# Kernel optimization log

Hardware: AMD Instinct MI355X
Metric: run time of the kernel (lower is better)

The kernel has to match this reference:

```python
import jax, jax.numpy as jnp
import numpy as np

NUM_LAYERS = 5
EMB_DIM = 300
NUM_ATOM_TYPE = 121
NUM_CHIRALITY = 11
NUM_BOND_TYPE = 7
NUM_BOND_DIR = 3
BN_EPS = 1e-5


def setup_inputs() -> dict:
    key = jax.random.key(0)
    ks = jax.random.split(key, 16)
    N, E, D, L = 100000, 200000, EMB_DIM, NUM_LAYERS

    def glorot(k, shape):
        fan_in, fan_out = shape[-2], shape[-1]
        s = jnp.sqrt(6.0 / (fan_in + fan_out))
        return jax.random.uniform(k, shape, jnp.float32, -s, s)

    x = jax.random.randint(ks[0], (N, 2), 0, 11)  # atom type / chirality (both < 11, in range)
    edge_index = jax.random.randint(ks[1], (2, E), 0, N)
    edge_attr = jax.random.randint(ks[2], (E, 2), 0, 3)

    return {
        "x": x,
        "edge_index": edge_index,
        "edge_attr": edge_attr,
        "x_emb1": glorot(ks[3], (NUM_ATOM_TYPE, D)),
        "x_emb2": glorot(ks[4], (NUM_CHIRALITY, D)),
        "edge_emb1": glorot(ks[5], (L, NUM_BOND_TYPE, D)),
        "edge_emb2": glorot(ks[6], (L, NUM_BOND_DIR, D)),
        "w1": glorot(ks[7], (L, D, 2 * D)),
        "b1": jnp.zeros((L, 2 * D), jnp.float32),
        "w2": glorot(ks[8], (L, 2 * D, D)),
        "b2": jnp.zeros((L, D), jnp.float32),
        "bn_gamma": jnp.ones((L, D), jnp.float32),
        "bn_beta": jnp.zeros((L, D), jnp.float32),
    }


def reference(x, edge_index, edge_attr, x_emb1, x_emb2, edge_emb1, edge_emb2,
              w1, b1, w2, b2, bn_gamma, bn_beta):
    N = x.shape[0]
    # GINConv.forward adds self loops with edge_attr row [4, 0]
    loop = jnp.arange(N)
    src = jnp.concatenate([edge_index[0], loop])  # [E+N]
    dst = jnp.concatenate([edge_index[1], loop])  # [E+N]
    ea0 = jnp.concatenate([edge_attr[:, 0], jnp.full((N,), 4, edge_attr.dtype)])
    ea1 = jnp.concatenate([edge_attr[:, 1], jnp.zeros((N,), edge_attr.dtype)])

    # node input embedding
    h = x_emb1[x[:, 0]] + x_emb2[x[:, 1]]  # [N, D]

    for l in range(NUM_LAYERS):
        # edge embeddings (incl. self loops)
        eemb = edge_emb1[l][ea0] + edge_emb2[l][ea1]  # [E+N, D]
        # message: x_j + edge_attr, aggr='add' at destination nodes
        msg = h[src] + eemb
        agg = jax.ops.segment_sum(msg, dst, num_segments=N)  # [N, D]
        # GIN update MLP: Linear(D, 2D) -> ReLU -> Linear(2D, D)
        h2 = jax.nn.relu(agg @ w1[l] + b1[l]) @ w2[l] + b2[l]
        # BatchNorm1d (training mode: batch statistics, biased variance)
        mean = h2.mean(axis=0)
        var = h2.var(axis=0)
        h2 = (h2 - mean) * jax.lax.rsqrt(var + BN_EPS) * bn_gamma[l] + bn_beta[l]
        # ReLU on all but last layer (dropout is identity, drop_ratio=0)
        if l < NUM_LAYERS - 1:
            h2 = jax.nn.relu(h2)
        h = h2
    # JK == 'last'
    return h
```

## Files before the change

### kernel.cpp

```cpp
#include <hip/hip_runtime.h>
#include <hip/hip_bf16.h>
#include <stdint.h>

typedef __bf16 bf16_t;
typedef bf16_t bf16x8 __attribute__((ext_vector_type(8)));
typedef bf16_t bf16x4 __attribute__((ext_vector_type(4)));
typedef float  f32x4  __attribute__((ext_vector_type(4)));

__global__ void embed_kernel(const int* __restrict__ x, const float* __restrict__ e1,
                             const float* __restrict__ e2, bf16_t* __restrict__ h, int N) {
  const int w = (blockIdx.x * blockDim.x + threadIdx.x) >> 6;
  const int lane = threadIdx.x & 63;
  if (w >= N || lane >= 40) return;
  const int t0 = x[2 * w], t1 = x[2 * w + 1];
  const int co = lane * 8;
  f32x4 a0 = *(const f32x4*)&e1[t0 * 300 + co];
  f32x4 a1 = *(const f32x4*)&e1[t0 * 300 + co + 4];
  f32x4 b0 = *(const f32x4*)&e2[t1 * 300 + co];
  f32x4 b1 = *(const f32x4*)&e2[t1 * 300 + co + 4];
  bf16x8 o;
  #pragma unroll
  for (int j = 0; j < 8; j++) {
    float v = (j < 4) ? (a0[j] + b0[j]) : (a1[j - 4] + b1[j - 4]);
    o[j] = (co + j < 300) ? (bf16_t)v : (bf16_t)0.f;
  }
  *(bf16x8*)&h[(size_t)w * 320 + co] = o;
}

__global__ void count_deg_kernel(const int* __restrict__ ei, int* __restrict__ deg, int E) {
  int e = blockIdx.x * 256 + threadIdx.x;
  if (e < E) atomicAdd(&deg[ei[E + e]], 1);
}

__global__ void scan_partial_kernel(const int* __restrict__ deg, int* __restrict__ part, int N) {
  __shared__ int s[256];
  const int tid = threadIdx.x;
  const int idx = blockIdx.x * 256 + tid;
  s[tid] = (idx < N) ? deg[idx] : 0;
  __syncthreads();
  for (int off = 128; off > 0; off >>= 1) {
    if (tid < off) s[tid] += s[tid + off];
    __syncthreads();
  }
  if (tid == 0) part[blockIdx.x] = s[0];
}

__global__ void scan_block_kernel(int* __restrict__ part, int n) {
  __shared__ int s[1024];
  const int tid = threadIdx.x;
  const int v = (tid < n) ? part[tid] : 0;
  s[tid] = v;
  __syncthreads();
  for (int off = 1; off < 1024; off <<= 1) {
    int x = (tid >= off) ? s[tid - off] : 0;
    __syncthreads();
    s[tid] += x;
    __syncthreads();
  }
  if (tid < n) part[tid] = s[tid] - v;
}

__global__ void scan_final_kernel(const int* __restrict__ deg, const int* __restrict__ part,
                                  int* __restrict__ rowptr, int* __restrict__ cursor, int N, int E) {
  __shared__ int s[256];
  const int tid = threadIdx.x;
  const int idx = blockIdx.x * 256 + tid;
  const int v = (idx < N) ? deg[idx] : 0;
  s[tid] = v;
  __syncthreads();
  for (int off = 1; off < 256; off <<= 1) {
    int x = (tid >= off) ? s[tid - off] : 0;
    __syncthreads();
    s[tid] += x;
    __syncthreads();
  }
  if (idx < N) {
    int ex = s[tid] - v + part[blockIdx.x];
    rowptr[idx] = ex;
    cursor[idx] = ex;
  }
  if (idx == 0) rowptr[N] = E;
}

__global__ void fill_csr_kernel(const int* __restrict__ ei, const int* __restrict__ ea,
                                int* __restrict__ cursor, int* __restrict__ epack, int E) {
  int e = blockIdx.x * 256 + threadIdx.x;
  if (e >= E) return;
  int slot = atomicAdd(&cursor[ei[E + e]], 1);
  int a = ea[2 * e] * 3 + ea[2 * e + 1];
  epack[slot] = (ei[e] & 0xFFFFF) | (a << 20);
}

__global__ void convert_w1_kernel(const float* __restrict__ w1, bf16_t* __restrict__ o) {
  int id = blockIdx.x * 256 + threadIdx.x;
  if (id >= 5 * 40 * 10 * 512) return;
  int j = id & 7;
  int lane = (id >> 3) & 63;
  int rest = id >> 9;
  int ks = rest % 10;
  int nt = (rest / 10) % 40;
  int l = rest / 400;
  int ml = lane & 15, quad = lane >> 4;
  int n = nt * 16 + ml;
  int k = ks * 32 + quad * 8 + j;
  float v = (k < 300 && n < 600) ? w1[((size_t)l * 300 + k) * 600 + n] : 0.f;
  o[id] = (bf16_t)v;
}

__global__ void convert_w2_kernel(const float* __restrict__ w2, bf16_t* __restrict__ o) {
  int id = blockIdx.x * 256 + threadIdx.x;
  if (id >= 5 * 24 * 20 * 512) return;
  int j = id & 7;
  int lane = (id >> 3) & 63;
  int rest = id >> 9;
  int ks = rest % 20;
  int nt = (rest / 20) % 24;
  int l = rest / 480;
  int ml = lane & 15, quad = lane >> 4;
  int n = nt * 16 + ml;
  int k = ks * 32 + quad * 8 + j;
  float v = (k < 600 && n < 300) ? w2[((size_t)l * 600 + k) * 300 + n] : 0.f;
  o[id] = (bf16_t)v;
}

__global__ void pad_bias_kernel(const float* __restrict__ b1, const float* __restrict__ b2,
                                float* __restrict__ b1p, float* __restrict__ b2p) {
  int t = blockIdx.x * 256 + threadIdx.x;
  if (t < 5 * 640) {
    int l = t / 640, n = t % 640;
    b1p[t] = (n < 600) ? b1[l * 600 + n] : 0.f;
  }
  if (t < 5 * 384) {
    int l = t / 384, n = t % 384;
    b2p[t] = (n < 300) ? b2[l * 300 + n] : 0.f;
  }
}

__global__ void build_t12_kernel(const float* __restrict__ ee1, const float* __restrict__ ee2,
                                 bf16_t* __restrict__ T12) {
  int id = blockIdx.x * 256 + threadIdx.x;
  if (id >= 5 * 21 * 320) return;
  int col = id % 320;
  int r = id / 320;
  int l = r / 21;
  int a = r % 21;
  int a0 = a / 3, a1 = a % 3;
  float v = 0.f;
  if (col < 300) v = ee1[((size_t)l * 7 + a0) * 300 + col] + ee2[((size_t)l * 3 + a1) * 300 + col];
  T12[id] = (bf16_t)v;
}

template <bool FUSE_BN>
__global__ void aggregate_kernel(const bf16_t* __restrict__ hsrc, const int* __restrict__ rowptr,
                                 const int* __restrict__ epack, const bf16_t* __restrict__ T12L,
                                 const float* __restrict__ scale, const float* __restrict__ shift,
                                 bf16_t* __restrict__ agg, int N, int LDH) {
  const int g = blockIdx.x * 256 + threadIdx.x;
  const int w = g / 40;
  if (w >= N) return;
  const int co = (g - w * 40) * 8;

  float sc[8], sh[8];
  if (FUSE_BN) {
    f32x4 s0 = *(const f32x4*)&scale[co];
    f32x4 s1 = *(const f32x4*)&scale[co + 4];
    f32x4 t0 = *(const f32x4*)&shift[co];
    f32x4 t1 = *(const f32x4*)&shift[co + 4];
    #pragma unroll
    for (int j = 0; j < 4; j++) { sc[j] = s0[j]; sc[j + 4] = s1[j]; sh[j] = t0[j]; sh[j + 4] = t1[j]; }
  }

  const int beg = rowptr[w], end = rowptr[w + 1];
  float acc[8];
  {
    bf16x8 hv = *(const bf16x8*)&hsrc[(size_t)w * LDH + co];
    bf16x8 tv = *(const bf16x8*)&T12L[12 * 320 + co];
    #pragma unroll
    for (int j = 0; j < 8; j++) {
      float v = (float)hv[j];
      if (FUSE_BN) v = fmaxf(v * sc[j] + sh[j], 0.f);
      acc[j] = v + (float)tv[j];
    }
  }
  for (int e = beg; e < end; e++) {
    const int p = epack[e];
    const int s = p & 0xFFFFF;
    const int a = (p >> 20) & 0x1F;
    bf16x8 hv = *(const bf16x8*)&hsrc[(size_t)s * LDH + co];
    bf16x8 tv = *(const bf16x8*)&T12L[a * 320 + co];
    #pragma unroll
    for (int j = 0; j < 8; j++) {
      float v = (float)hv[j];
      if (FUSE_BN) v = fmaxf(v * sc[j] + sh[j], 0.f);
      acc[j] += v + (float)tv[j];
    }
  }
  bf16x8 o;
  #pragma unroll
  for (int j = 0; j < 8; j++) o[j] = (bf16_t)acc[j];
  *(bf16x8*)&agg[(size_t)w * 320 + co] = o;
}

__global__ __launch_bounds__(512) void fused_mlp_kernel(
    const bf16_t* __restrict__ agg,
    const bf16_t* __restrict__ W1f,
    const bf16_t* __restrict__ W2f,
    const float* __restrict__ b1p,
    const float* __restrict__ b2p,
    bf16_t* __restrict__ H2,
    float* __restrict__ sums, float* __restrict__ sumsq, int Nvalid) {
  __shared__ __align__(16) bf16_t As[10 * 64 * 32];
  __shared__ __align__(16) bf16_t C1p[64 * 136];

  const int tid = threadIdx.x;
  const int lane = tid & 63;
  const int w = tid >> 6;
  const int ml = lane & 15, quad = lane >> 4;
  const int kx = (ml >> 1) & 3;
  const size_t bm = (size_t)blockIdx.x * 64;

  #pragma unroll
  for (int it = 0; it < 5; it++) {
    const int s = it * 512 + tid;
    const int ks = s >> 8;
    const int u = s & 255;
    const int row = u >> 2;
    const int cg = (u & 3) ^ ((u >> 3) & 3);
    bf16x8 v = *(const bf16x8*)&agg[(bm + row) * 320 + ks * 32 + cg * 8];
    *(bf16x8*)&As[(size_t)s * 8] = v;
  }
  asm volatile("s_waitcnt lgkmcnt(0)" ::: "memory");
  __builtin_amdgcn_s_barrier();

  f32x4 acc1[4];
  f32x4 acc2[4][3];
  #pragma unroll
  for (int mf = 0; mf < 4; mf++)
    #pragma unroll
    for (int nf = 0; nf < 3; nf++) acc2[mf][nf] = (f32x4){0.f, 0.f, 0.f, 0.f};

  auto phase1 = [&](int c) {
    #pragma unroll
    for (int mt = 0; mt < 4; mt++) acc1[mt] = (f32x4){0.f, 0.f, 0.f, 0.f};
    const bf16_t* wp = W1f + (((size_t)(c * 8 + w) * 10) * 64 + lane) * 8;
    #pragma unroll
    for (int ks = 0; ks < 10; ks++) {
      bf16x8 w1f = *(const bf16x8*)(wp + (size_t)ks * 512);
      #pragma unroll
      for (int mt = 0; mt < 4; mt++) {
        bf16x8 aF = *(const bf16x8*)&As[((ks * 64 + mt * 16 + ml) * 4 + (quad ^ kx)) * 8];
        acc1[mt] = __builtin_amdgcn_mfma_f32_16x16x32_bf16(w1f, aF, acc1[mt], 0, 0, 0);
      }
    }
  };

  phase1(0);

  for (int c = 0; c < 5; c++) {
    {
      const int nloc = w * 16 + quad * 4;
      f32x4 bv = *(const f32x4*)&b1p[c * 128 + nloc];
      #pragma unroll
      for (int mt = 0; mt < 4; mt++) {
        bf16x4 o;
        #pragma unroll
        for (int i = 0; i < 4; i++) {
          float v = acc1[mt][i] + bv[i];
          o[i] = (bf16_t)fmaxf(v, 0.f);
        }
        *(bf16x4*)&C1p[(mt * 16 + ml) * 136 + nloc] = o;
      }
    }
    asm volatile("s_waitcnt lgkmcnt(0)" ::: "memory");
    __builtin_amdgcn_s_barrier();

    #pragma unroll
    for (int ks2 = 0; ks2 < 4; ks2++) {
      bf16x8 c1f[4];
      #pragma unroll
      for (int mf = 0; mf < 4; mf++)
        c1f[mf] = *(const bf16x8*)&C1p[(mf * 16 + ml) * 136 + ks2 * 32 + quad * 8];
      #pragma unroll
      for (int nf = 0; nf < 3; nf++) {
        bf16x8 w2f = *(const bf16x8*)&W2f[(((size_t)(w * 3 + nf) * 20 + c * 4 + ks2) * 64 + lane) * 8];
        #pragma unroll
        for (int mf = 0; mf < 4; mf++)
          acc2[mf][nf] = __builtin_amdgcn_mfma_f32_16x16x32_bf16(c1f[mf], w2f, acc2[mf][nf], 0, 0, 0);
      }
    }
    if (c < 4) phase1(c + 1);
    asm volatile("s_waitcnt lgkmcnt(0)" ::: "memory");
    __builtin_amdgcn_s_barrier();
  }

  #pragma unroll
  for (int nf = 0; nf < 3; nf++) {
    const int colg = (w * 3 + nf) * 16 + ml;
    const float bv = b2p[colg];
    float s = 0.f, sq = 0.f;
    #pragma unroll
    for (int mf = 0; mf < 4; mf++) {
      #pragma unroll
      for (int i = 0; i < 4; i++) {
        const size_t rowg = bm + mf * 16 + quad * 4 + i;
        float v = acc2[mf][nf][i] + bv;
        H2[rowg * 384 + colg] = (bf16_t)v;
        const bool ok = rowg < (size_t)Nvalid;
        s += ok ? v : 0.f;
        sq += ok ? v * v : 0.f;
      }
    }
    s += __shfl_down(s, 16);
    sq += __shfl_down(sq, 16);
    s += __shfl_down(s, 32);
    sq += __shfl_down(sq, 32);
    if (quad == 0) {
      atomicAdd(&sums[colg], s);
      atomicAdd(&sumsq[colg], sq);
    }
  }
}

__global__ void bn_params_kernel(const float* __restrict__ sums, const float* __restrict__ sumsq,
                                 const float* __restrict__ gamma, const float* __restrict__ beta,
                                 float* __restrict__ scale, float* __restrict__ shift, int N) {
  const int col = threadIdx.x;
  if (col >= 384) return;
  if (col >= 300) {
    scale[col] = 0.f;
    shift[col] = 0.f;
    return;
  }
  const float inv = 1.f / (float)N;
  const float mean = sums[col] * inv;
  float var = sumsq[col] * inv - mean * mean;
  if (var < 0.f) var = 0.f;
  const float sc = gamma[col] * rsqrtf(var + 1e-5f);
  scale[col] = sc;
  shift[col] = beta[col] - mean * sc;
}

__global__ void bn_apply_kernel(const bf16_t* __restrict__ H2, const float* __restrict__ scale,
                                const float* __restrict__ shift, float* __restrict__ out, int N) {
  const int w = (blockIdx.x * blockDim.x + threadIdx.x) >> 6;
  const int lane = threadIdx.x & 63;
  if (w >= N || lane >= 40) return;
  const int co = lane * 8;
  bf16x8 v8 = *(const bf16x8*)&H2[(size_t)w * 384 + co];
  f32x4 s0 = *(const f32x4*)&scale[co];
  f32x4 s1 = *(const f32x4*)&scale[co + 4];
  f32x4 t0 = *(const f32x4*)&shift[co];
  f32x4 t1 = *(const f32x4*)&shift[co + 4];
  #pragma unroll
  for (int j = 0; j < 8; j++) {
    float sc = (j < 4) ? s0[j] : s1[j - 4];
    float sh = (j < 4) ? t0[j] : t1[j - 4];
    float v = (float)v8[j] * sc + sh;
    if (co + j < 300) out[(size_t)w * 300 + co + j] = v;
  }
}

extern "C" void kernel_launch(void* const* d_in, const int* in_sizes, int n_in,
                              void* d_out, int out_size, void* d_ws, size_t ws_size,
                              hipStream_t stream) {
  const int* x = (const int*)d_in[0];
  const int* ei = (const int*)d_in[1];
  const int* ea = (const int*)d_in[2];
  const float* xe1 = (const float*)d_in[3];
  const float* xe2 = (const float*)d_in[4];
  const float* ee1 = (const float*)d_in[5];
  const float* ee2 = (const float*)d_in[6];
  const float* w1 = (const float*)d_in[7];
  const float* b1 = (const float*)d_in[8];
  const float* w2 = (const float*)d_in[9];
  const float* b2 = (const float*)d_in[10];
  const float* gam = (const float*)d_in[11];
  const float* bet = (const float*)d_in[12];

  const int N = in_sizes[0] / 2;
  const int E = in_sizes[1] / 2;
  const int Mt = (N + 127) / 128;
  const size_t Mp = (size_t)Mt * 128;
  const int Mt2 = (int)(Mp / 64);

  char* p = (char*)d_ws;
  auto take = [&](size_t b) -> char* {
    char* r = p;
    p += (b + 255) & ~(size_t)255;
    return r;
  };
  bf16_t* h    = (bf16_t*)take(Mp * 320 * 2);
  bf16_t* agg  = (bf16_t*)take(Mp * 320 * 2);
  bf16_t* H2   = (bf16_t*)take(Mp * 384 * 2);
  bf16_t* W1f  = (bf16_t*)take((size_t)5 * 40 * 10 * 512 * 2);
  bf16_t* W2f  = (bf16_t*)take((size_t)5 * 24 * 20 * 512 * 2);
  bf16_t* T12  = (bf16_t*)take((size_t)5 * 21 * 320 * 2);
  float* b1p   = (float*)take((size_t)5 * 640 * 4);
  float* b2p   = (float*)take((size_t)5 * 384 * 4);
  int* deg     = (int*)take((size_t)N * 4);
  int* rowptr  = (int*)take((size_t)(N + 1) * 4);
  int* cursor  = (int*)take((size_t)N * 4);
  int* part    = (int*)take(1024 * 4);
  int* epack   = (int*)take((size_t)E * 4);
  float* sums  = (float*)take(384 * 4);
  float* sumsq = (float*)take(384 * 4);
  float* scale = (float*)take(384 * 4);
  float* shift = (float*)take(384 * 4);

  hipMemsetAsync(agg, 0, Mp * 320 * 2, stream);
  hipMemsetAsync(deg, 0, (size_t)N * 4, stream);

  const int nwb = (N + 3) / 4;
  embed_kernel<<<nwb, 256, 0, stream>>>(x, xe1, xe2, h, N);

  count_deg_kernel<<<(E + 255) / 256, 256, 0, stream>>>(ei, deg, E);
  const int nsb = (N + 255) / 256;
  scan_partial_kernel<<<nsb, 256, 0, stream>>>(deg, part, N);
  scan_block_kernel<<<1, 1024, 0, stream>>>(part, nsb);
  scan_final_kernel<<<nsb, 256, 0, stream>>>(deg, part, rowptr, cursor, N, E);
  fill_csr_kernel<<<(E + 255) / 256, 256, 0, stream>>>(ei, ea, cursor, epack, E);

  convert_w1_kernel<<<(5 * 40 * 10 * 512 + 255) / 256, 256, 0, stream>>>(w1, W1f);
  convert_w2_kernel<<<(5 * 24 * 20 * 512 + 255) / 256, 256, 0, stream>>>(w2, W2f);
  pad_bias_kernel<<<(5 * 640 + 255) / 256, 256, 0, stream>>>(b1, b2, b1p, b2p);
  build_t12_kernel<<<(5 * 21 * 320 + 255) / 256, 256, 0, stream>>>(ee1, ee2, T12);

  const int nab = (N * 40 + 255) / 256;

  for (int l = 0; l < 5; l++) {
    if (l == 0) {
      aggregate_kernel<false><<<nab, 256, 0, stream>>>(h, rowptr, epack,
                                                       T12 + (size_t)l * 21 * 320,
                                                       scale, shift, agg, N, 320);
    } else {
      aggregate_kernel<true><<<nab, 256, 0, stream>>>(H2, rowptr, epack,
                                                      T12 + (size_t)l * 21 * 320,
                                                      scale, shift, agg, N, 384);
    }
    hipMemsetAsync(sums, 0, 384 * 4, stream);
    hipMemsetAsync(sumsq, 0, 384 * 4, stream);
    fused_mlp_kernel<<<Mt2, 512, 0, stream>>>(
        agg, W1f + (size_t)l * 40 * 10 * 512, W2f + (size_t)l * 24 * 20 * 512,
        b1p + (size_t)l * 640, b2p + (size_t)l * 384, H2, sums, sumsq, N);
    bn_params_kernel<<<1, 384, 0, stream>>>(sums, sumsq, gam + (size_t)l * 300,
                                            bet + (size_t)l * 300, scale, shift, N);
  }
  bn_apply_kernel<<<nwb, 256, 0, stream>>>(H2, scale, shift, (float*)d_out, N);
}
```

Measured before the change: 1.384 ms.

## Double-buffer MLP hidden tile and retile phase1 with XOR-swizzled LDS

The fused MLP kernel now keeps two hidden-activation buffers in LDS, so phase1 for chunk c+1 writes one buffer while phase2 reads the other. This removes one barrier per chunk. Phase1 is retiled so each wave computes a 2x2 block of 16x16 tiles (two row groups by four column groups), which reuses each W1 fragment load across two A fragments. The padded C1 layout is replaced with an XOR swizzle to avoid LDS bank conflicts, and launch bounds now request 4 waves per SIMD. The second buffer adds LDS, and the occupancy hint may cause register spills.

After: 1.300 ms. -6.1%, faster.

```diff
diff --git a/kernel.cpp b/kernel.cpp
--- a/kernel.cpp
+++ b/kernel.cpp
@@ -201,7 +201,7 @@
   *(bf16x8*)&agg[(size_t)w * 320 + co] = o;
 }
 
-__global__ __launch_bounds__(512) void fused_mlp_kernel(
+__global__ __launch_bounds__(512, 4) void fused_mlp_kernel(
     const bf16_t* __restrict__ agg,
     const bf16_t* __restrict__ W1f,
     const bf16_t* __restrict__ W2f,
@@ -210,13 +210,16 @@
     bf16_t* __restrict__ H2,
     float* __restrict__ sums, float* __restrict__ sumsq, int Nvalid) {
   __shared__ __align__(16) bf16_t As[10 * 64 * 32];
-  __shared__ __align__(16) bf16_t C1p[64 * 136];
+  __shared__ __align__(16) bf16_t C1pA[64 * 128];
+  __shared__ __align__(16) bf16_t C1pB[64 * 128];
 
   const int tid = threadIdx.x;
   const int lane = tid & 63;
   const int w = tid >> 6;
   const int ml = lane & 15, quad = lane >> 4;
   const int kx = (ml >> 1) & 3;
+  const int k7 = ml & 7;
+  const int rg = w >> 2, cg = w & 3;
   const size_t bm = (size_t)blockIdx.x * 64;
 
   #pragma unroll
@@ -225,61 +228,65 @@
     const int ks = s >> 8;
     const int u = s & 255;
     const int row = u >> 2;
-    const int cg = (u & 3) ^ ((u >> 3) & 3);
-    bf16x8 v = *(const bf16x8*)&agg[(bm + row) * 320 + ks * 32 + cg * 8];
+    const int cgl = (u & 3) ^ ((u >> 3) & 3);
+    bf16x8 v = *(const bf16x8*)&agg[(bm + row) * 320 + ks * 32 + cgl * 8];
     *(bf16x8*)&As[(size_t)s * 8] = v;
   }
   asm volatile("s_waitcnt lgkmcnt(0)" ::: "memory");
   __builtin_amdgcn_s_barrier();
-
-  f32x4 acc1[4];
+  __builtin_amdgcn_sched_barrier(0);
+
   f32x4 acc2[4][3];
   #pragma unroll
   for (int mf = 0; mf < 4; mf++)
     #pragma unroll
     for (int nf = 0; nf < 3; nf++) acc2[mf][nf] = (f32x4){0.f, 0.f, 0.f, 0.f};
 
-  auto phase1 = [&](int c) {
-    #pragma unroll
-    for (int mt = 0; mt < 4; mt++) acc1[mt] = (f32x4){0.f, 0.f, 0.f, 0.f};
-    const bf16_t* wp = W1f + (((size_t)(c * 8 + w) * 10) * 64 + lane) * 8;
+  auto phase1 = [&](int c, bf16_t* dst) {
+    f32x4 a1[2][2];
+    #pragma unroll
+    for (int mi = 0; mi < 2; mi++)
+      #pragma unroll
+      for (int ni = 0; ni < 2; ni++) a1[mi][ni] = (f32x4){0.f, 0.f, 0.f, 0.f};
+    const int nt0 = c * 8 + cg * 2;
     #pragma unroll
     for (int ks = 0; ks < 10; ks++) {
-      bf16x8 w1f = *(const bf16x8*)(wp + (size_t)ks * 512);
-      #pragma unroll
-      for (int mt = 0; mt < 4; mt++) {
-        bf16x8 aF = *(const bf16x8*)&As[((ks * 64 + mt * 16 + ml) * 4 + (quad ^ kx)) * 8];
-        acc1[mt] = __builtin_amdgcn_mfma_f32_16x16x32_bf16(w1f, aF, acc1[mt], 0, 0, 0);
+      bf16x8 w1f0 = *(const bf16x8*)&W1f[(((size_t)nt0 * 10 + ks) * 64 + lane) * 8];
+      bf16x8 w1f1 = *(const bf16x8*)&W1f[(((size_t)(nt0 + 1) * 10 + ks) * 64 + lane) * 8];
+      #pragma unroll
+      for (int mi = 0; mi < 2; mi++) {
+        bf16x8 aF = *(const bf16x8*)&As[((ks * 64 + rg * 32 + mi * 16 + ml) * 4 + (quad ^ kx)) * 8];
+        a1[mi][0] = __builtin_amdgcn_mfma_f32_16x16x32_bf16(w1f0, aF, a1[mi][0], 0, 0, 0);
+        a1[mi][1] = __builtin_amdgcn_mfma_f32_16x16x32_bf16(w1f1, aF, a1[mi][1], 0, 0, 0);
       }
     }
-  };
-
-  phase1(0);
-
-  for (int c = 0; c < 5; c++) {
-    {
-      const int nloc = w * 16 + quad * 4;
-      f32x4 bv = *(const f32x4*)&b1p[c * 128 + nloc];
-      #pragma unroll
-      for (int mt = 0; mt < 4; mt++) {
+    #pragma unroll
+    for (int mi = 0; mi < 2; mi++) {
+      const int row = rg * 32 + mi * 16 + ml;
+      #pragma unroll
+      for (int ni = 0; ni < 2; ni++) {
+        const int colb = cg * 32 + ni * 16 + quad * 4;
+        f32x4 bv = *(const f32x4*)&b1p[c * 128 + colb];
         bf16x4 o;
         #pragma unroll
-        for (int i = 0; i < 4; i++) {
-          float v = acc1[mt][i] + bv[i];
-          o[i] = (bf16_t)fmaxf(v, 0.f);
-        }
-        *(bf16x4*)&C1p[(mt * 16 + ml) * 136 + nloc] = o;
+        for (int i = 0; i < 4; i++) o[i] = (bf16_t)fmaxf(a1[mi][ni][i] + bv[i], 0.f);
+        const int ls = colb >> 3;
+        const int off = colb & 7;
+        *(bf16x4*)&dst[row * 128 + ((ls ^ k7) * 8) + off] = o;
       }
     }
-    asm volatile("s_waitcnt lgkmcnt(0)" ::: "memory");
-    __builtin_amdgcn_s_barrier();
-
+  };
+
+  auto phase2 = [&](int c, const bf16_t* src) {
     #pragma unroll
     for (int ks2 = 0; ks2 < 4; ks2++) {
       bf16x8 c1f[4];
       #pragma unroll
-      for (int mf = 0; mf < 4; mf++)
-        c1f[mf] = *(const bf16x8*)&C1p[(mf * 16 + ml) * 136 + ks2 * 32 + quad * 8];
+      for (int mf = 0; mf < 4; mf++) {
+        const int row = mf * 16 + ml;
+        const int ls = ks2 * 4 + quad;
+        c1f[mf] = *(const bf16x8*)&src[row * 128 + ((ls ^ k7) * 8)];
+      }
       #pragma unroll
       for (int nf = 0; nf < 3; nf++) {
         bf16x8 w2f = *(const bf16x8*)&W2f[(((size_t)(w * 3 + nf) * 20 + c * 4 + ks2) * 64 + lane) * 8];
@@ -288,9 +295,22 @@
           acc2[mf][nf] = __builtin_amdgcn_mfma_f32_16x16x32_bf16(c1f[mf], w2f, acc2[mf][nf], 0, 0, 0);
       }
     }
-    if (c < 4) phase1(c + 1);
+  };
+
+  phase1(0, C1pA);
+  asm volatile("s_waitcnt lgkmcnt(0)" ::: "memory");
+  __builtin_amdgcn_s_barrier();
+  __builtin_amdgcn_sched_barrier(0);
+
+  #pragma unroll
+  for (int c = 0; c < 5; c++) {
+    bf16_t* cur = (c & 1) ? C1pB : C1pA;
+    bf16_t* oth = (c & 1) ? C1pA : C1pB;
+    if (c < 4) phase1(c + 1, oth);
+    phase2(c, cur);
     asm volatile("s_waitcnt lgkmcnt(0)" ::: "memory");
     __builtin_amdgcn_s_barrier();
+    __builtin_amdgcn_sched_barrier(0);
   }
 
   #pragma unroll
```
